# Kernel optimization log

Measured on AMD Instinct MI355X. Metric: run time of the kernel, lower is better.

The kernel has to match this reference:

```python
import jax, jax.numpy as jnp
import numpy as np

N_NODES = 50000
N_EDGES = 640000
N_F = 128
E_F = 128
U_F = 64
HIDDEN = 256
N_GRAPHS = 64


def setup_inputs() -> dict:
    key = jax.random.key(0)
    ks = jax.random.split(key, 12)
    s = 0.02
    x = jax.random.normal(ks[0], (N_NODES, N_F), dtype=jnp.float32)
    edge_index = jax.random.randint(ks[1], (2, N_EDGES), 0, N_NODES, dtype=jnp.int64)
    edge_attr = jax.random.normal(ks[2], (N_EDGES, E_F), dtype=jnp.float32)
    u = jax.random.normal(ks[3], (N_GRAPHS, U_F), dtype=jnp.float32)
    batch = jnp.sort(jax.random.randint(ks[4], (N_NODES,), 0, N_GRAPHS, dtype=jnp.int64))
    # node_mlp_1: Lin(n_f+e_f, hidden) -> ReLU -> Lin(hidden, hidden)
    W1 = jax.random.normal(ks[5], (N_F + E_F, HIDDEN), dtype=jnp.float32) * s
    b1 = jnp.zeros((HIDDEN,), dtype=jnp.float32)
    W2 = jax.random.normal(ks[6], (HIDDEN, HIDDEN), dtype=jnp.float32) * s
    b2 = jnp.zeros((HIDDEN,), dtype=jnp.float32)
    # node_mlp_2: Lin(n_f+hidden+u_f, hidden) -> ReLU -> Lin(hidden, n_f)
    W3 = jax.random.normal(ks[7], (N_F + HIDDEN + U_F, HIDDEN), dtype=jnp.float32) * s
    b3 = jnp.zeros((HIDDEN,), dtype=jnp.float32)
    W4 = jax.random.normal(ks[8], (HIDDEN, N_F), dtype=jnp.float32) * s
    b4 = jnp.zeros((N_F,), dtype=jnp.float32)
    return {"x": x, "edge_index": edge_index, "edge_attr": edge_attr, "u": u,
            "batch": batch, "W1": W1, "b1": b1, "W2": W2, "b2": b2,
            "W3": W3, "b3": b3, "W4": W4, "b4": b4}


def scatter_mean(src, index, dim_size):
    summed = jax.ops.segment_sum(src, index, num_segments=dim_size)
    counts = jax.ops.segment_sum(jnp.ones((src.shape[0],), dtype=src.dtype), index,
                                 num_segments=dim_size)
    return summed / jnp.maximum(counts, 1.0)[:, None]


def reference(x, edge_index, edge_attr, u, batch, W1, b1, W2, b2, W3, b3, W4, b4):
    row, col = edge_index[0], edge_index[1]
    # edge-wise MLP on [x[row] || edge_attr]  -> [E, hidden]
    h = jnp.concatenate([x[row], edge_attr], axis=1)
    h = jax.nn.relu(h @ W1 + b1) @ W2 + b2
    # aggregate messages to destination nodes (mean)
    agg = scatter_mean(h, col, dim_size=x.shape[0])  # [N, hidden]
    # node-wise MLP on [x || agg || u[batch]]
    z = jnp.concatenate([x, agg, u[batch]], axis=1)
    return jax.nn.relu(z @ W3 + b3) @ W4 + b4  # [N, n_f]
```

## Files before the change

### kernel.cpp

```cpp
#include <hip/hip_runtime.h>

#define NNODES 50000
#define NEDGES 640000
#define NF 128
#define EF 128
#define UF 64
#define HID 256
#define ZK 448
#define NSCANB 196

typedef float floatx4 __attribute__((ext_vector_type(4)));
typedef __bf16 bf16x8 __attribute__((ext_vector_type(8)));

__device__ __forceinline__ unsigned short f2bf(float f) {
    unsigned int u = __float_as_uint(f);
    u += 0x7fffu + ((u >> 16) & 1u);
    return (unsigned short)(u >> 16);
}

__device__ __forceinline__ float bf2f(unsigned short h) {
    return __uint_as_float(((unsigned int)h) << 16);
}

__global__ void kconv_t(const float* __restrict__ w, unsigned short* __restrict__ wt,
                        int K, int N) {
    int i = blockIdx.x * 256 + threadIdx.x;
    if (i >= K * N) return;
    int n = i / K, k = i - n * K;
    wt[i] = f2bf(w[(size_t)k * N + n]);
}

__global__ void kxb(const float* __restrict__ x, unsigned short* __restrict__ xb) {
    int i = blockIdx.x * 256 + threadIdx.x;
    if (i >= NNODES * NF / 4) return;
    float4 v = *(const float4*)(x + (size_t)i * 4);
    unsigned lo = (unsigned)f2bf(v.x) | ((unsigned)f2bf(v.y) << 16);
    unsigned hi = (unsigned)f2bf(v.z) | ((unsigned)f2bf(v.w) << 16);
    *(uint2*)&xb[(size_t)i * 4] = make_uint2(lo, hi);
}

__global__ void kfold_w(const float* __restrict__ W2, const float* __restrict__ W3,
                        unsigned short* __restrict__ W3tp) {
    const int k = blockIdx.x;
    const int n = threadIdx.x;
    float v;
    if (k < NF || k >= NF + HID) {
        v = W3[(size_t)k * HID + n];
    } else {
        const int j = k - NF;
        float s = 0.f;
        for (int c = 0; c < HID; ++c)
            s += W2[(size_t)j * HID + c] * W3[(size_t)(NF + c) * HID + n];
        v = s;
    }
    W3tp[(size_t)n * ZK + k] = f2bf(v);
}

__global__ void kfold_b(const float* __restrict__ b2, const float* __restrict__ b3,
                        const float* __restrict__ W3, float* __restrict__ b3p) {
    const int n = threadIdx.x;
    float s = b3[n];
    for (int c = 0; c < HID; ++c)
        s += b2[c] * W3[(size_t)(NF + c) * HID + n];
    b3p[n] = s;
}

__global__ void kcount(const int* __restrict__ eidx, int* __restrict__ cnt) {
    int i = blockIdx.x * 256 + threadIdx.x;
    if (i < NEDGES) atomicAdd(&cnt[eidx[NEDGES + i]], 1);
}

__global__ void kscan1(const int* __restrict__ cnt, int* __restrict__ excl,
                       int* __restrict__ btot) {
    __shared__ int s[256];
    const int t = threadIdx.x, i = blockIdx.x * 256 + t;
    int v = (i < NNODES) ? cnt[i] : 0;
    s[t] = v;
    __syncthreads();
    for (int off = 1; off < 256; off <<= 1) {
        int add = (t >= off) ? s[t - off] : 0;
        __syncthreads();
        s[t] += add;
        __syncthreads();
    }
    if (i < NNODES) excl[i] = s[t] - v;
    if (t == 255) btot[blockIdx.x] = s[255];
}

__global__ void kscan2(int* __restrict__ btot) {
    __shared__ int s[256];
    const int t = threadIdx.x;
    int v = (t < NSCANB) ? btot[t] : 0;
    s[t] = v;
    __syncthreads();
    for (int off = 1; off < 256; off <<= 1) {
        int add = (t >= off) ? s[t - off] : 0;
        __syncthreads();
        s[t] += add;
        __syncthreads();
    }
    if (t < NSCANB) btot[t] = s[t] - v;
}

__global__ void kstart(const int* __restrict__ cnt, const int* __restrict__ excl,
                       const int* __restrict__ btot, int* __restrict__ head,
                       float* __restrict__ inv) {
    int i = blockIdx.x * 256 + threadIdx.x;
    if (i >= NNODES) return;
    head[i] = excl[i] + btot[blockIdx.x];
    int c = cnt[i];
    inv[i] = 1.0f / (float)(c > 1 ? c : 1);
}

__global__ void kscatter(const int* __restrict__ eidx, int* __restrict__ head,
                         uint2* __restrict__ osd) {
    int e = blockIdx.x * 256 + threadIdx.x;
    if (e < NEDGES) {
        int d = eidx[NEDGES + e];
        int p = atomicAdd(&head[d], 1);
        osd[p] = make_uint2((unsigned)e, (unsigned)d);
    }
}

#define ESE2 264
#define SZ_BYTES (128 * ESE2 * 2)
#define SMEM_BYTES (SZ_BYTES + 3 * 128 * 4)

__device__ __forceinline__ int sid128(int r) {
    return (((r >> 2) & 3) << 5) + ((r >> 4) << 2) + (r & 3);
}

__global__ __launch_bounds__(512, 4)
void kscat(const float* __restrict__ ea, const unsigned short* __restrict__ xb,
           const int* __restrict__ eidx, const uint2* __restrict__ osd,
           const unsigned short* __restrict__ W1t,
           const float* __restrict__ b1, float* __restrict__ agg) {
    extern __shared__ char smem[];
    unsigned short* sZ = (unsigned short*)smem;
    int* sRow = (int*)(smem + SZ_BYTES);
    int* sCol = (int*)(smem + SZ_BYTES + 512);
    int* sOrd = (int*)(smem + SZ_BYTES + 1024);
    const int tid = threadIdx.x;
    const int vb = (blockIdx.x & 7) * 625 + (blockIdx.x >> 3);
    const int e0 = vb * 128;

    if (tid < 128) {
        uint2 od = osd[e0 + tid];
        sOrd[tid] = (int)od.x;
        sCol[tid] = (int)od.y;
        sRow[tid] = eidx[od.x];
    }
    __syncthreads();

    #pragma unroll
    for (int i = 0; i < 4; ++i) {
        int c2 = i * 512 + tid;
        int r = c2 >> 4, ch = c2 & 15;
        uint4 v = *(const uint4*)(xb + (size_t)sRow[sid128(r)] * NF + ch * 8);
        *(uint4*)&sZ[r * ESE2 + ch * 8] = v;
    }
    #pragma unroll
    for (int i = 0; i < 8; ++i) {
        int lin = (i << 11) + (tid << 2);
        int r = lin >> 7, c = lin & 127;
        float4 v = *(const float4*)(ea + (size_t)sOrd[sid128(r)] * EF + c);
        unsigned lo = (unsigned)f2bf(v.x) | ((unsigned)f2bf(v.y) << 16);
        unsigned hi = (unsigned)f2bf(v.z) | ((unsigned)f2bf(v.w) << 16);
        *(uint2*)&sZ[r * ESE2 + NF + c] = make_uint2(lo, hi);
    }
    __syncthreads();

    const int lane = tid & 63, wave = tid >> 6;
    const int l16 = lane & 15, quad = lane >> 4;
    const int nbase = wave * 32;
    const floatx4 fz = {0.f, 0.f, 0.f, 0.f};

    floatx4 acc[8][2];
    #pragma unroll
    for (int mi = 0; mi < 8; ++mi) {
        acc[mi][0] = fz;
        acc[mi][1] = fz;
    }

    #pragma unroll
    for (int ks = 0; ks < 8; ++ks) {
        const int k0 = ks * 32 + quad * 8;
        bf16x8 b0 = *(const bf16x8*)&W1t[(size_t)(nbase + l16) * HID + k0];
        bf16x8 b1v = *(const bf16x8*)&W1t[(size_t)(nbase + 16 + l16) * HID + k0];
        #pragma unroll
        for (int mi = 0; mi < 8; ++mi) {
            bf16x8 a = *(const bf16x8*)&sZ[(mi * 16 + l16) * ESE2 + k0];
            acc[mi][0] = __builtin_amdgcn_mfma_f32_16x16x32_bf16(a, b0, acc[mi][0], 0, 0, 0);
            acc[mi][1] = __builtin_amdgcn_mfma_f32_16x16x32_bf16(a, b1v, acc[mi][1], 0, 0, 0);
        }
    }

    #pragma unroll
    for (int ni = 0; ni < 2; ++ni) {
        const int n = nbase + ni * 16 + l16;
        const float bias = b1[n];
        const int sbase = quad * 32;
        int d0 = sCol[sbase];
        float s = 0.f;
        #pragma unroll
        for (int mi = 0; mi < 8; ++mi)
            #pragma unroll
            for (int r = 0; r < 4; ++r) {
                const float h = fmaxf(acc[mi][ni][r] + bias, 0.f);
                const int d = sCol[sbase + mi * 4 + r];
                if (d != d0) {
                    unsafeAtomicAdd(&agg[(size_t)d0 * HID + n], s);
                    d0 = d; s = 0.f;
                }
                s += h;
            }
        unsafeAtomicAdd(&agg[(size_t)d0 * HID + n], s);
    }
}

#define ZST 456

__global__ __launch_bounds__(256)
void knode(const float* __restrict__ x, const float* __restrict__ agg,
           const float* __restrict__ inv, const float* __restrict__ u,
           const int* __restrict__ batch,
           const unsigned short* __restrict__ W3t, const float* __restrict__ b3,
           const unsigned short* __restrict__ W4t, const float* __restrict__ b4,
           float* __restrict__ out) {
    __shared__ unsigned short sZ[64 * ZST];
    const int tid = threadIdx.x;
    const int n0 = blockIdx.x * 64;

    {
        const int r = tid >> 2, q = tid & 3;
        const int nc = min(n0 + r, NNODES - 1);
        const float invv = inv[nc];
        const int bg = batch[nc];
        for (int j = 0; j < 28; ++j) {
            const int c = q * 112 + (j << 2);
            float4 v;
            if (c < NF) {
                v = *(const float4*)(x + (size_t)nc * NF + c);
            } else if (c < NF + HID) {
                v = *(const float4*)(agg + (size_t)nc * HID + (c - NF));
                v.x *= invv; v.y *= invv; v.z *= invv; v.w *= invv;
            } else {
                v = *(const float4*)(u + (size_t)bg * UF + (c - NF - HID));
            }
            unsigned lo = (unsigned)f2bf(v.x) | ((unsigned)f2bf(v.y) << 16);
            unsigned hi = (unsigned)f2bf(v.z) | ((unsigned)f2bf(v.w) << 16);
            *(uint2*)&sZ[r * ZST + c] = make_uint2(lo, hi);
        }
    }
    __syncthreads();

    const int lane = tid & 63, wave = tid >> 6;
    const int l16 = lane & 15, quad = lane >> 4;
    const floatx4 fz = {0.f, 0.f, 0.f, 0.f};

    {
        const int nbase = wave * 64;
        floatx4 acc[4][4];
        #pragma unroll
        for (int mi = 0; mi < 4; ++mi)
            #pragma unroll
            for (int ni = 0; ni < 4; ++ni) acc[mi][ni] = fz;

        #pragma unroll 2
        for (int ks = 0; ks < 14; ++ks) {
            const int k0 = ks * 32 + quad * 8;
            bf16x8 a[4], b[4];
            #pragma unroll
            for (int mi = 0; mi < 4; ++mi)
                a[mi] = *(const bf16x8*)&sZ[(mi * 16 + l16) * ZST + k0];
            #pragma unroll
            for (int ni = 0; ni < 4; ++ni)
                b[ni] = *(const bf16x8*)&W3t[(size_t)(nbase + ni * 16 + l16) * ZK + k0];
            #pragma unroll
            for (int mi = 0; mi < 4; ++mi)
                #pragma unroll
                for (int ni = 0; ni < 4; ++ni)
                    acc[mi][ni] = __builtin_amdgcn_mfma_f32_16x16x32_bf16(a[mi], b[ni], acc[mi][ni], 0, 0, 0);
        }
        __syncthreads();
        #pragma unroll
        for (int ni = 0; ni < 4; ++ni) {
            const int n = nbase + ni * 16 + l16;
            const float bias = b3[n];
            #pragma unroll
            for (int mi = 0; mi < 4; ++mi)
                #pragma unroll
                for (int r = 0; r < 4; ++r) {
                    const int row = mi * 16 + quad * 4 + r;
                    sZ[row * ZST + n] = f2bf(fmaxf(acc[mi][ni][r] + bias, 0.f));
                }
        }
        __syncthreads();
    }

    {
        const int nbase = wave * 32;
        floatx4 acc[4][2];
        #pragma unroll
        for (int mi = 0; mi < 4; ++mi)
            #pragma unroll
            for (int ni = 0; ni < 2; ++ni) acc[mi][ni] = fz;

        #pragma unroll 2
        for (int ks = 0; ks < 8; ++ks) {
            const int k0 = ks * 32 + quad * 8;
            bf16x8 a[4], b[2];
            #pragma unroll
            for (int mi = 0; mi < 4; ++mi)
                a[mi] = *(const bf16x8*)&sZ[(mi * 16 + l16) * ZST + k0];
            #pragma unroll
            for (int ni = 0; ni < 2; ++ni)
                b[ni] = *(const bf16x8*)&W4t[(size_t)(nbase + ni * 16 + l16) * HID + k0];
            #pragma unroll
            for (int mi = 0; mi < 4; ++mi)
                #pragma unroll
                for (int ni = 0; ni < 2; ++ni)
                    acc[mi][ni] = __builtin_amdgcn_mfma_f32_16x16x32_bf16(a[mi], b[ni], acc[mi][ni], 0, 0, 0);
        }
        #pragma unroll
        for (int ni = 0; ni < 2; ++ni) {
            const int feat = nbase + ni * 16 + l16;
            const float bias = b4[feat];
            #pragma unroll
            for (int mi = 0; mi < 4; ++mi)
                #pragma unroll
                for (int r = 0; r < 4; ++r) {
                    const int row = mi * 16 + quad * 4 + r;
                    const int n = n0 + row;
                    if (n < NNODES)
                        out[(size_t)n * NF + feat] = acc[mi][ni][r] + bias;
                }
        }
    }
}

extern "C" void kernel_launch(void* const* d_in, const int* in_sizes, int n_in,
                              void* d_out, int out_size, void* d_ws, size_t ws_size,
                              hipStream_t stream) {
    const float* x   = (const float*)d_in[0];
    const int*   ei  = (const int*)d_in[1];
    const float* ea  = (const float*)d_in[2];
    const float* u   = (const float*)d_in[3];
    const int*   bat = (const int*)d_in[4];
    const float* W1  = (const float*)d_in[5];
    const float* b1  = (const float*)d_in[6];
    const float* W2  = (const float*)d_in[7];
    const float* b2  = (const float*)d_in[8];
    const float* W3  = (const float*)d_in[9];
    const float* b3  = (const float*)d_in[10];
    const float* W4  = (const float*)d_in[11];
    const float* b4  = (const float*)d_in[12];
    float* out = (float*)d_out;

    char* p = (char*)d_ws;
    float* agg = (float*)p;                   p += (size_t)NNODES * HID * 4;
    int* cnt   = (int*)p;                     p += (size_t)NNODES * 4;
    float* inv = (float*)p;                   p += (size_t)NNODES * 4;
    int* excl  = (int*)p;                     p += (size_t)NNODES * 4;
    int* btot  = (int*)p;                     p += 256 * 4;
    int* head  = (int*)p;                     p += (size_t)NNODES * 4;
    uint2* osd = (uint2*)p;                   p += (size_t)NEDGES * 8;
    unsigned short* xb  = (unsigned short*)p; p += (size_t)NNODES * NF * 2;
    unsigned short* W1t = (unsigned short*)p; p += (size_t)HID * HID * 2;
    unsigned short* W3tp= (unsigned short*)p; p += (size_t)ZK * HID * 2;
    unsigned short* W4t = (unsigned short*)p; p += (size_t)HID * NF * 2;
    float* b3p = (float*)p;                   p += (size_t)HID * 4;

    hipMemsetAsync(agg, 0, (size_t)NNODES * HID * 4, stream);
    hipMemsetAsync(cnt, 0, (size_t)NNODES * 4, stream);

    kconv_t<<<(HID * HID + 255) / 256, 256, 0, stream>>>(W1, W1t, HID, HID);
    kconv_t<<<(HID * NF + 255) / 256, 256, 0, stream>>>(W4, W4t, HID, NF);
    kxb<<<(NNODES * NF / 4 + 255) / 256, 256, 0, stream>>>(x, xb);
    kfold_w<<<ZK, 256, 0, stream>>>(W2, W3, W3tp);
    kfold_b<<<1, 256, 0, stream>>>(b2, b3, W3, b3p);

    kcount<<<(NEDGES + 255) / 256, 256, 0, stream>>>(ei, cnt);
    kscan1<<<NSCANB, 256, 0, stream>>>(cnt, excl, btot);
    kscan2<<<1, 256, 0, stream>>>(btot);
    kstart<<<NSCANB, 256, 0, stream>>>(cnt, excl, btot, head, inv);
    kscatter<<<(NEDGES + 255) / 256, 256, 0, stream>>>(ei, head, osd);

    static bool attr_set = false;
    if (!attr_set) {
        hipFuncSetAttribute((const void*)kscat,
                            hipFuncAttributeMaxDynamicSharedMemorySize, SMEM_BYTES);
        attr_set = true;
    }
    kscat<<<NEDGES / 128, 512, SMEM_BYTES, stream>>>(ea, xb, ei, osd, W1t, b1, agg);
    knode<<<(NNODES + 63) / 64, 256, 0, stream>>>(x, agg, inv, u, bat, W3tp, b3p, W4t, b4, out);
}
```

Measured before the change: 794.6 us.

## Replace per-run atomics with plain stores, merging segment boundaries across lanes and blocks

The edge-MLP scatter kernel now sums sorted-destination runs inside each lane. Runs wholly inside the block are written with plain stores instead of atomic adds. Partial head and tail sums from the four 32-row lane groups are gathered with shuffles and merged when a destination spans groups. Atomics are kept only where a destination crosses into the neighbouring block, detected from new prev/next destination lookups. This cuts global atomic traffic to agg but adds branchy boundary logic and relies on agg being zeroed beforehand and on the sorted order being correct.

```diff
diff --git a/kernel.cpp b/kernel.cpp
--- a/kernel.cpp
+++ b/kernel.cpp
@@ -124,7 +124,7 @@
 
 #define ESE2 264
 #define SZ_BYTES (128 * ESE2 * 2)
-#define SMEM_BYTES (SZ_BYTES + 3 * 128 * 4)
+#define SMEM_BYTES (SZ_BYTES + 3 * 128 * 4 + 8)
 
 __device__ __forceinline__ int sid128(int r) {
     return (((r >> 2) & 3) << 5) + ((r >> 4) << 2) + (r & 3);
@@ -140,6 +140,7 @@
     int* sRow = (int*)(smem + SZ_BYTES);
     int* sCol = (int*)(smem + SZ_BYTES + 512);
     int* sOrd = (int*)(smem + SZ_BYTES + 1024);
+    int* sPN  = (int*)(smem + SZ_BYTES + 1536);
     const int tid = threadIdx.x;
     const int vb = (blockIdx.x & 7) * 625 + (blockIdx.x >> 3);
     const int e0 = vb * 128;
@@ -149,6 +150,8 @@
         sOrd[tid] = (int)od.x;
         sCol[tid] = (int)od.y;
         sRow[tid] = eidx[od.x];
+        if (tid == 0) sPN[0] = (vb > 0) ? (int)osd[e0 - 1].y : -1;
+        if (tid == 1) sPN[1] = (vb < NEDGES / 128 - 1) ? (int)osd[e0 + 128].y : -1;
     }
     __syncthreads();
 
@@ -195,26 +198,138 @@
         }
     }
 
-    #pragma unroll
-    for (int ni = 0; ni < 2; ++ni) {
-        const int n = nbase + ni * 16 + l16;
-        const float bias = b1[n];
-        const int sbase = quad * 32;
+    const int sbase = quad * 32;
+    const int Da0 = sCol[0],   Da1 = sCol[31];
+    const int Db0 = sCol[32],  Db1 = sCol[63];
+    const int Dc0 = sCol[64],  Dc1 = sCol[95];
+    const int Dd0 = sCol[96],  Dd1 = sCol[127];
+    const bool sg0 = (Da0 == Da1), sg1 = (Db0 == Db1),
+               sg2 = (Dc0 == Dc1), sg3 = (Dd0 == Dd1);
+    const bool lk0 = (Da1 == Db0), lk1 = (Db1 == Dc0), lk2 = (Dc1 == Dd0);
+    const int prevD = sPN[0], nextD = sPN[1];
+
+    const int n0c = nbase + l16;
+    const int n1c = nbase + 16 + l16;
+    const float bias0 = b1[n0c];
+    const float bias1 = b1[n1c];
+
+    float s0 = 0.f, s1 = 0.f, hs0 = 0.f, hs1 = 0.f;
+    {
         int d0 = sCol[sbase];
-        float s = 0.f;
+        bool headOpen = true;
         #pragma unroll
         for (int mi = 0; mi < 8; ++mi)
             #pragma unroll
             for (int r = 0; r < 4; ++r) {
-                const float h = fmaxf(acc[mi][ni][r] + bias, 0.f);
-                const int d = sCol[sbase + mi * 4 + r];
+                const int p = mi * 4 + r;
+                const float h0 = fmaxf(acc[mi][0][r] + bias0, 0.f);
+                const float h1 = fmaxf(acc[mi][1][r] + bias1, 0.f);
+                const int d = sCol[sbase + p];
                 if (d != d0) {
-                    unsafeAtomicAdd(&agg[(size_t)d0 * HID + n], s);
-                    d0 = d; s = 0.f;
+                    if (headOpen) {
+                        hs0 = s0; hs1 = s1; headOpen = false;
+                    } else {
+                        agg[(size_t)d0 * HID + n0c] = s0;
+                        agg[(size_t)d0 * HID + n1c] = s1;
+                    }
+                    d0 = d; s0 = 0.f; s1 = 0.f;
                 }
-                s += h;
-            }
-        unsafeAtomicAdd(&agg[(size_t)d0 * HID + n], s);
+                s0 += h0; s1 += h1;
+            }
+    }
+
+    float tA0 = __shfl(s0, l16, 64),      tA1 = __shfl(s1, l16, 64);
+    float tB0 = __shfl(s0, l16 + 16, 64), tB1 = __shfl(s1, l16 + 16, 64);
+    float tC0 = __shfl(s0, l16 + 32, 64), tC1 = __shfl(s1, l16 + 32, 64);
+    float tD0 = __shfl(s0, l16 + 48, 64), tD1 = __shfl(s1, l16 + 48, 64);
+    float hA0 = __shfl(hs0, l16, 64),      hA1 = __shfl(hs1, l16, 64);
+    float hB0 = __shfl(hs0, l16 + 16, 64), hB1 = __shfl(hs1, l16 + 16, 64);
+    float hC0 = __shfl(hs0, l16 + 32, 64), hC1 = __shfl(hs1, l16 + 32, 64);
+    float hD0 = __shfl(hs0, l16 + 48, 64), hD1 = __shfl(hs1, l16 + 48, 64);
+
+    if (quad == 0) {
+        if (!sg0) {
+            if (Da0 == prevD) {
+                unsafeAtomicAdd(&agg[(size_t)Da0 * HID + n0c], hA0);
+                unsafeAtomicAdd(&agg[(size_t)Da0 * HID + n1c], hA1);
+            } else {
+                agg[(size_t)Da0 * HID + n0c] = hA0;
+                agg[(size_t)Da0 * HID + n1c] = hA1;
+            }
+        }
+        {
+            float c0 = tA0, c1 = tA1;
+            bool stop = false; int endSeg = 0;
+            if (lk0) { if (sg1) { c0 += tB0; c1 += tB1; endSeg = 1; }
+                       else     { c0 += hB0; c1 += hB1; stop = true; } }
+            if (!stop && endSeg == 1 && lk1) {
+                if (sg2) { c0 += tC0; c1 += tC1; endSeg = 2; }
+                else     { c0 += hC0; c1 += hC1; stop = true; } }
+            if (!stop && endSeg == 2 && lk2) {
+                if (sg3) { c0 += tD0; c1 += tD1; endSeg = 3; }
+                else     { c0 += hD0; c1 += hD1; stop = true; } }
+            const bool lx = sg0 && (Da0 == prevD);
+            const bool rx = (!stop && endSeg == 3) && (Dd1 == nextD);
+            if (lx || rx) {
+                unsafeAtomicAdd(&agg[(size_t)Da1 * HID + n0c], c0);
+                unsafeAtomicAdd(&agg[(size_t)Da1 * HID + n1c], c1);
+            } else {
+                agg[(size_t)Da1 * HID + n0c] = c0;
+                agg[(size_t)Da1 * HID + n1c] = c1;
+            }
+        }
+        if (!sg1 || !lk0) {
+            if (!sg1 && !lk0) {
+                agg[(size_t)Db0 * HID + n0c] = hB0;
+                agg[(size_t)Db0 * HID + n1c] = hB1;
+            }
+            float c0 = tB0, c1 = tB1;
+            bool stop = false; int endSeg = 1;
+            if (lk1) { if (sg2) { c0 += tC0; c1 += tC1; endSeg = 2; }
+                       else     { c0 += hC0; c1 += hC1; stop = true; } }
+            if (!stop && endSeg == 2 && lk2) {
+                if (sg3) { c0 += tD0; c1 += tD1; endSeg = 3; }
+                else     { c0 += hD0; c1 += hD1; stop = true; } }
+            const bool rx = (!stop && endSeg == 3) && (Dd1 == nextD);
+            if (rx) {
+                unsafeAtomicAdd(&agg[(size_t)Db1 * HID + n0c], c0);
+                unsafeAtomicAdd(&agg[(size_t)Db1 * HID + n1c], c1);
+            } else {
+                agg[(size_t)Db1 * HID + n0c] = c0;
+                agg[(size_t)Db1 * HID + n1c] = c1;
+            }
+        }
+        if (!sg2 || !lk1) {
+            if (!sg2 && !lk1) {
+                agg[(size_t)Dc0 * HID + n0c] = hC0;
+                agg[(size_t)Dc0 * HID + n1c] = hC1;
+            }
+            float c0 = tC0, c1 = tC1;
+            bool stop = false; int endSeg = 2;
+            if (lk2) { if (sg3) { c0 += tD0; c1 += tD1; endSeg = 3; }
+                       else     { c0 += hD0; c1 += hD1; stop = true; } }
+            const bool rx = (!stop && endSeg == 3) && (Dd1 == nextD);
+            if (rx) {
+                unsafeAtomicAdd(&agg[(size_t)Dc1 * HID + n0c], c0);
+                unsafeAtomicAdd(&agg[(size_t)Dc1 * HID + n1c], c1);
+            } else {
+                agg[(size_t)Dc1 * HID + n0c] = c0;
+                agg[(size_t)Dc1 * HID + n1c] = c1;
+            }
+        }
+        if (!sg3 || !lk2) {
+            if (!sg3 && !lk2) {
+                agg[(size_t)Dd0 * HID + n0c] = hD0;
+                agg[(size_t)Dd0 * HID + n1c] = hD1;
+            }
+            if (Dd1 == nextD) {
+                unsafeAtomicAdd(&agg[(size_t)Dd1 * HID + n0c], tD0);
+                unsafeAtomicAdd(&agg[(size_t)Dd1 * HID + n1c], tD1);
+            } else {
+                agg[(size_t)Dd1 * HID + n0c] = tD0;
+                agg[(size_t)Dd1 * HID + n1c] = tD1;
+            }
+        }
     }
 }
 
```

After: 812.4 us. 2.2% more time.
